# Optimization experiments

Hardware: AMD Instinct MI355X
Metric: run time of the kernel (lower is better)

Reference implementation:

```python
import jax, jax.numpy as jnp
import numpy as np

DIM = 768
HEADS = 12
HEAD_DIM = DIM // HEADS
SCALE = HEAD_DIM ** (-0.5)
GAMMA_INIT = 1.0


def _split_heads(x, B, H, Dh):
    # [B, N, C] -> [B, H, N, Dh]
    return x.reshape(B, -1, H, Dh).transpose(0, 2, 1, 3)


def setup_inputs() -> dict:
    key = jax.random.key(0)
    ks = jax.random.split(key, 10)
    B, N, C = 4, 1024, DIM
    w = lambda k: jax.random.normal(k, (C, C), dtype=jnp.float32) * 0.02
    return {
        "fc": jax.random.normal(ks[0], (B, N, C), dtype=jnp.float32),
        "fs": jax.random.normal(ks[1], (B, N, C), dtype=jnp.float32),
        "Wqc": w(ks[2]),
        "Wqs": w(ks[3]),
        "Wkc": w(ks[4]),
        "Wvc": w(ks[5]),
        "Wvs": w(ks[6]),
        "gamma": jnp.ones((HEADS,), dtype=jnp.float32) * GAMMA_INIT,
        "Wpc": w(ks[7]),
        "bpc": jnp.zeros((C,), dtype=jnp.float32),
        "Wps": w(ks[8]),
        "bps": jnp.zeros((C,), dtype=jnp.float32),
    }


def reference(fc, fs, Wqc, Wqs, Wkc, Wvc, Wvs, gamma, Wpc, bpc, Wps, bps):
    B, N, C = fc.shape
    H, Dh = HEADS, HEAD_DIM
    sg = jax.lax.stop_gradient

    qc = _split_heads(fc @ Wqc, B, H, Dh)
    qs = _split_heads(fs @ Wqs, B, H, Dh)
    kc = _split_heads(fc @ Wkc, B, H, Dh)
    vc = _split_heads(fc @ Wvc, B, H, Dh)
    vs = _split_heads(fs @ Wvs, B, H, Dh)

    # content attention: standard scaled QK^T
    attn_c = jnp.einsum("bhnd,bhmd->bhnm", qc, kc) * SCALE
    # semantic attention: L2-normalized self-similarity, per-head gamma
    qs_n = qs / jnp.linalg.norm(qs, axis=-1, keepdims=True)
    attn_s = jnp.einsum("bhnd,bhmd->bhnm", qs_n, qs_n) * gamma[None, :, None, None]

    # double softmax: identical forward values, asymmetric stop-gradients
    attn1 = jax.nn.softmax(attn_c + sg(attn_s), axis=-1)
    attn2 = jax.nn.softmax(sg(attn_c) + attn_s, axis=-1)

    oc = jnp.einsum("bhnm,bhmd->bhnd", attn1, vc).transpose(0, 2, 1, 3).reshape(B, N, C)
    os_ = jnp.einsum("bhnm,bhmd->bhnd", attn2, vs).transpose(0, 2, 1, 3).reshape(B, N, C)

    out_c = oc @ Wpc + bpc
    out_s = os_ @ Wps + bps
    return (out_c, out_s)
```

## Files before the change

kernel.cpp:

```cpp
#include <hip/hip_runtime.h>
#include <cstdint>
#include <cstddef>

#define DEV __device__ __forceinline__

typedef __bf16 v8bf __attribute__((ext_vector_type(8)));
typedef float v4f __attribute__((ext_vector_type(4)));
typedef float f32x16 __attribute__((ext_vector_type(16)));
typedef uint16_t u16;

DEV u16 f2bf(float f) {
    union { __bf16 b; u16 u; } cv;
    cv.b = (__bf16)f;
    return cv.u;
}
DEV float bf2f(u16 h) { return __uint_as_float((uint32_t)h << 16); }

DEV uint32_t pkbf(float a, float b) {
    typedef __bf16 bf2v __attribute__((ext_vector_type(2)));
    union { bf2v v; uint32_t u; } c;
    c.v = (bf2v){(__bf16)a, (__bf16)b};
    return c.u;
}

DEV void gload16(void* lds, const void* g) {
    __builtin_amdgcn_global_load_lds(
        (const __attribute__((address_space(1))) unsigned int*)g,
        (__attribute__((address_space(3))) unsigned int*)lds, 16, 0, 0);
}

DEV void wait_vm0() {
    asm volatile("s_waitcnt vmcnt(0)" ::: "memory");
    __builtin_amdgcn_sched_barrier(0);
}

__global__ __launch_bounds__(256) void k_cvt2(const float* __restrict__ a, const float* __restrict__ b,
                                              u16* __restrict__ da, u16* __restrict__ db) {
    const float* s = blockIdx.y ? b : a;
    u16* d = blockIdx.y ? db : da;
    int i = blockIdx.x * 256 + threadIdx.x;
    float4 v = reinterpret_cast<const float4*>(s)[i];
    ushort4 o;
    o.x = f2bf(v.x); o.y = f2bf(v.y); o.z = f2bf(v.z); o.w = f2bf(v.w);
    reinterpret_cast<ushort4*>(d)[i] = o;
}

__global__ __launch_bounds__(256) void k_transpose_w(
    const float* __restrict__ w0, const float* __restrict__ w1, const float* __restrict__ w2,
    const float* __restrict__ w3, const float* __restrict__ w4, const float* __restrict__ w5,
    const float* __restrict__ w6, u16* __restrict__ Wt) {
    __shared__ float tl[32][33];
    const float* W;
    switch (blockIdx.z) {
        case 0: W = w0; break; case 1: W = w1; break; case 2: W = w2; break;
        case 3: W = w3; break; case 4: W = w4; break; case 5: W = w5; break;
        default: W = w6; break;
    }
    int n0 = blockIdx.x * 32, k0 = blockIdx.y * 32;
    int tx = threadIdx.x & 31, ty = threadIdx.x >> 5;
    #pragma unroll
    for (int i = 0; i < 4; ++i)
        tl[ty + i*8][tx] = W[(size_t)(k0 + ty + i*8) * 768 + n0 + tx];
    __syncthreads();
    u16* O = Wt + (size_t)blockIdx.z * 589824;
    #pragma unroll
    for (int i = 0; i < 4; ++i)
        O[(size_t)(n0 + ty + i*8) * 768 + k0 + tx] = f2bf(tl[tx][ty + i*8]);
}

DEV void gemm_main(const u16* __restrict__ A, const u16* __restrict__ W,
                   u16* As, u16* Bs, int m0, int n0, v4f acc[4][4]) {
    const int t = threadIdx.x, lane = t & 63;
    const int wid = t >> 6, wm = wid >> 1, wn = wid & 1;
    const int lr = lane & 15, kg = lane >> 4;
    const int lrow = lane >> 3, lslot = lane & 7;
    const int s = lslot ^ lrow;
    #pragma unroll
    for (int mi = 0; mi < 4; ++mi)
        #pragma unroll
        for (int ni = 0; ni < 4; ++ni) acc[mi][ni] = (v4f){0.f, 0.f, 0.f, 0.f};
    for (int kt = 0; kt < 12; ++kt) {
        int k0 = kt * 64;
        #pragma unroll
        for (int c = 0; c < 4; ++c) {
            int rb = wid * 32 + c * 8;
            int r = rb + lrow;
            gload16((char*)As + rb * 128, A + (size_t)(m0 + r) * 768 + k0 + s * 8);
            gload16((char*)Bs + rb * 128, W + (size_t)(n0 + r) * 768 + k0 + s * 8);
        }
        __syncthreads();
        #pragma unroll
        for (int kk = 0; kk < 2; ++kk) {
            int kb2 = (kk * 32 + kg * 8) * 2;
            v8bf af[4], bfr[4];
            #pragma unroll
            for (int mi = 0; mi < 4; ++mi) {
                int rr = wm * 64 + mi * 16 + lr;
                af[mi] = *reinterpret_cast<const v8bf*>(reinterpret_cast<const char*>(As) + rr * 128 + (kb2 ^ ((rr & 7) << 4)));
            }
            #pragma unroll
            for (int ni = 0; ni < 4; ++ni) {
                int rr = wn * 64 + ni * 16 + lr;
                bfr[ni] = *reinterpret_cast<const v8bf*>(reinterpret_cast<const char*>(Bs) + rr * 128 + (kb2 ^ ((rr & 7) << 4)));
            }
            #pragma unroll
            for (int mi = 0; mi < 4; ++mi)
                #pragma unroll
                for (int ni = 0; ni < 4; ++ni)
                    acc[mi][ni] = __builtin_amdgcn_mfma_f32_16x16x32_bf16(af[mi], bfr[ni], acc[mi][ni], 0, 0, 0);
        }
        __syncthreads();
    }
}

__global__ __launch_bounds__(256) void k_gemm_proj(
    const u16* __restrict__ fcb, const u16* __restrict__ fsb, const u16* __restrict__ Wt,
    u16* __restrict__ qc, u16* __restrict__ kc, u16* __restrict__ vc,
    u16* __restrict__ qs, u16* __restrict__ vs) {
    __shared__ __align__(16) u16 As[8192], Bs[8192];
    const u16* A; const u16* W; u16* O;
    switch (blockIdx.z) {
        case 0:  A = fcb; W = Wt;              O = qc; break;
        case 1:  A = fcb; W = Wt + 589824;     O = kc; break;
        case 2:  A = fcb; W = Wt + 2 * 589824; O = vc; break;
        case 3:  A = fsb; W = Wt + 3 * 589824; O = qs; break;
        default: A = fsb; W = Wt + 4 * 589824; O = vs; break;
    }
    int m0 = blockIdx.y * 128, n0 = blockIdx.x * 128;
    v4f acc[4][4];
    gemm_main(A, W, As, Bs, m0, n0, acc);
    const int lane = threadIdx.x & 63, wid = threadIdx.x >> 6;
    const int wm = wid >> 1, wn = wid & 1, lr = lane & 15, kg = lane >> 4;
    if (blockIdx.z == 0) {
        #pragma unroll
        for (int mi = 0; mi < 4; ++mi)
            #pragma unroll
            for (int ni = 0; ni < 4; ++ni)
                #pragma unroll
                for (int r = 0; r < 4; ++r) acc[mi][ni][r] *= 0.18033688f;
    } else if (blockIdx.z == 3) {
        #pragma unroll
        for (int mi = 0; mi < 4; ++mi)
            #pragma unroll
            for (int r = 0; r < 4; ++r) {
                float ss = 0.f;
                #pragma unroll
                for (int ni = 0; ni < 4; ++ni) ss += acc[mi][ni][r] * acc[mi][ni][r];
                ss += __shfl_xor(ss, 1); ss += __shfl_xor(ss, 2);
                ss += __shfl_xor(ss, 4); ss += __shfl_xor(ss, 8);
                float rs = rsqrtf(ss);
                #pragma unroll
                for (int ni = 0; ni < 4; ++ni) acc[mi][ni][r] *= rs;
            }
    }
    #pragma unroll
    for (int mi = 0; mi < 4; ++mi)
        #pragma unroll
        for (int ni = 0; ni < 4; ++ni)
            #pragma unroll
            for (int r = 0; r < 4; ++r) {
                int rowg = m0 + wm * 64 + mi * 16 + kg * 4 + r;
                int colg = n0 + wn * 64 + ni * 16 + lr;
                O[(size_t)rowg * 768 + colg] = f2bf(acc[mi][ni][r]);
            }
}

__global__ __launch_bounds__(256) void k_gemm_out(
    const u16* __restrict__ ocb, const u16* __restrict__ osb, const u16* __restrict__ Wt,
    const float* __restrict__ bpc, const float* __restrict__ bps, float* __restrict__ out) {
    __shared__ __align__(16) u16 As[8192], Bs[8192];
    const u16* A; const u16* W; const float* bias; float* O;
    if (blockIdx.z == 0) { A = ocb; W = Wt + 5 * 589824; bias = bpc; O = out; }
    else                 { A = osb; W = Wt + 6 * 589824; bias = bps; O = out + 3145728; }
    int m0 = blockIdx.y * 128, n0 = blockIdx.x * 128;
    v4f acc[4][4];
    gemm_main(A, W, As, Bs, m0, n0, acc);
    const int lane = threadIdx.x & 63, wid = threadIdx.x >> 6;
    const int wm = wid >> 1, wn = wid & 1, lr = lane & 15, kg = lane >> 4;
    #pragma unroll
    for (int mi = 0; mi < 4; ++mi)
        #pragma unroll
        for (int ni = 0; ni < 4; ++ni)
            #pragma unroll
            for (int r = 0; r < 4; ++r) {
                int rowg = m0 + wm * 64 + mi * 16 + kg * 4 + r;
                int colg = n0 + wn * 64 + ni * 16 + lr;
                O[(size_t)rowg * 768 + colg] = acc[mi][ni][r] + bias[colg];
            }
}

__global__ __launch_bounds__(256) void k_transpose_v(
    const u16* __restrict__ vc, const u16* __restrict__ vs,
    u16* __restrict__ vcT, u16* __restrict__ vsT) {
    __shared__ u16 tile[64][65];
    const u16* src = blockIdx.z ? vs : vc;
    u16* dst = blockIdx.z ? vsT : vcT;
    int bh = blockIdx.y, b = bh / 12, h = bh % 12;
    int n0 = blockIdx.x * 64;
    int t = threadIdx.x;
    #pragma unroll
    for (int i = 0; i < 16; ++i) {
        int idx = i * 256 + t, n = idx >> 6, d = idx & 63;
        tile[n][d] = src[(size_t)(b * 1024 + n0 + n) * 768 + h * 64 + d];
    }
    __syncthreads();
    #pragma unroll
    for (int i = 0; i < 16; ++i) {
        int idx = i * 256 + t, d = idx >> 6, n = idx & 63;
        dst[(size_t)(bh * 64 + d) * 1024 + n0 + n] = tile[n][d];
    }
}

__global__ __launch_bounds__(256, 2) void k_attn(
    const u16* __restrict__ qc, const u16* __restrict__ kc, const u16* __restrict__ qsn,
    const u16* __restrict__ vcT, const u16* __restrict__ vsT,
    const float* __restrict__ gamma,
    u16* __restrict__ oc, u16* __restrict__ os) {
    __shared__ __align__(16) u16 SH[24576];
    u16* K_s8  = SH;
    u16* Q2_s8 = SH + 4096;
    u16* Vb    = SH + 8192;
    const int t = threadIdx.x, lane = t & 63, w = t >> 6;
    const int lq = lane & 31, hf = lane >> 5;
    const int qg = w >> 1, kvh = w & 1;
    const int lrow = lane >> 3, lslot = lane & 7;
    const int sslot = lslot ^ lrow;

    int lin = blockIdx.y * 16 + blockIdx.x;
    int swz = (lin & 7) * 96 + (lin >> 3);
    const int qb = swz & 15, bh = swz >> 4;
    const int b = bh / 12, h = bh % 12;
    const float gam = gamma[h] * 1.44269504088896340736f;

    const u16* gb; size_t rstride, kmul;
    switch (w) {
        case 0:  gb = kc  + (size_t)b * 786432 + h * 64; rstride = 768;  kmul = 768; break;
        case 1:  gb = qsn + (size_t)b * 786432 + h * 64; rstride = 768;  kmul = 768; break;
        case 2:  gb = vcT + (size_t)bh * 65536;          rstride = 1024; kmul = 1;   break;
        default: gb = vsT + (size_t)bh * 65536;          rstride = 1024; kmul = 1;   break;
    }
    u16* fixdst = (w == 0) ? K_s8 : Q2_s8;

    const u16* qp1 = qc  + (size_t)(b * 1024 + qb * 64 + qg * 32 + lq) * 768 + h * 64 + hf * 8;
    const u16* qp2 = qsn + (size_t)(b * 1024 + qb * 64 + qg * 32 + lq) * 768 + h * 64 + hf * 8;
    v8bf qcB[4], qsB[4];
    #pragma unroll
    for (int s = 0; s < 4; ++s) {
        qcB[s] = *reinterpret_cast<const v8bf*>(qp1 + s * 16);
        qsB[s] = *reinterpret_cast<const v8bf*>(qp2 + s * 16);
    }

    f32x16 ocA[2], osA[2];
    #pragma unroll
    for (int dt = 0; dt < 2; ++dt) {
        #pragma unroll
        for (int r = 0; r < 16; ++r) { ocA[dt][r] = 0.f; osA[dt][r] = 0.f; }
    }
    float lsum = 0.f;

    {
        char* ld = (w < 2) ? (char*)fixdst : (char*)(Vb + (w - 2) * 4096);
        #pragma unroll
        for (int c = 0; c < 8; ++c) {
            int r = c * 8 + lrow;
            gload16(ld + c * 1024, gb + (size_t)r * rstride + sslot * 8);
        }
    }
    wait_vm0();
    __builtin_amdgcn_s_barrier();

    int cur = 0;
    for (int tile = 0; tile < 16; ++tile) {
        if (tile < 15 && w >= 2) {
            size_t kv1 = (size_t)(tile + 1) * 64;
            char* ld = (char*)(Vb + ((cur ^ 1) * 2 + (w - 2)) * 4096);
            #pragma unroll
            for (int c = 0; c < 8; ++c) {
                int r = c * 8 + lrow;
                gload16(ld + c * 1024, gb + kv1 * kmul + (size_t)r * rstride + sslot * 8);
            }
        }
        const char* K_s  = (const char*)K_s8;
        const char* Q2_s = (const char*)Q2_s8;
        const char* Vc_s = (const char*)(Vb + (cur * 2 + 0) * 4096);
        const char* Vs_s = (const char*)(Vb + (cur * 2 + 1) * 4096);

        f32x16 ac, as;
        #pragma unroll
        for (int r = 0; r < 16; ++r) { ac[r] = 0.f; as[r] = 0.f; }
        const int rowA = kvh * 32 + lq;
        __builtin_amdgcn_s_setprio(1);
        #pragma unroll
        for (int s = 0; s < 4; ++s) {
            int colb = s * 32 + hf * 16;
            int off = rowA * 128 + (colb ^ ((rowA & 7) << 4));
            v8bf kf  = *reinterpret_cast<const v8bf*>(K_s + off);
            v8bf q2f = *reinterpret_cast<const v8bf*>(Q2_s + off);
            ac = __builtin_amdgcn_mfma_f32_32x32x16_bf16(kf,  qcB[s], ac, 0, 0, 0);
            as = __builtin_amdgcn_mfma_f32_32x32x16_bf16(q2f, qsB[s], as, 0, 0, 0);
        }
        __builtin_amdgcn_s_setprio(0);

        __builtin_amdgcn_s_barrier();
        if (tile < 15 && w < 2) {
            size_t kv1 = (size_t)(tile + 1) * 64;
            #pragma unroll
            for (int c = 0; c < 8; ++c) {
                int r = c * 8 + lrow;
                gload16((char*)fixdst + c * 1024, gb + kv1 * kmul + (size_t)r * rstride + sslot * 8);
            }
        }

        float p[16];
        #pragma unroll
        for (int r = 0; r < 16; ++r)
            p[r] = __builtin_exp2f(fmaf(gam, as[r], ac[r]));
        lsum += ((p[0]+p[1])+(p[2]+p[3])) + ((p[4]+p[5])+(p[6]+p[7]))
              + ((p[8]+p[9])+(p[10]+p[11])) + ((p[12]+p[13])+(p[14]+p[15]));

        uint32_t A0 = pkbf(p[0], p[1]),  A1 = pkbf(p[2], p[3]);
        uint32_t A2 = pkbf(p[4], p[5]),  A3 = pkbf(p[6], p[7]);
        uint32_t A4 = pkbf(p[8], p[9]),  A5 = pkbf(p[10], p[11]);
        uint32_t A6 = pkbf(p[12], p[13]), A7 = pkbf(p[14], p[15]);
        uint32_t pay0 = hf ? A0 : A2;
        uint32_t pay1 = hf ? A1 : A3;
        uint32_t rec0 = (uint32_t)__shfl_xor((int)pay0, 32);
        uint32_t rec1 = (uint32_t)__shfl_xor((int)pay1, 32);
        uint32_t w0 = hf ? rec0 : A0;
        uint32_t w1 = hf ? rec1 : A1;
        uint32_t w2 = hf ? A2 : rec0;
        uint32_t w3 = hf ? A3 : rec1;
        uint32_t pay2 = hf ? A4 : A6;
        uint32_t pay3 = hf ? A5 : A7;
        uint32_t rec2 = (uint32_t)__shfl_xor((int)pay2, 32);
        uint32_t rec3 = (uint32_t)__shfl_xor((int)pay3, 32);
        uint32_t w4 = hf ? rec2 : A4;
        uint32_t w5 = hf ? rec3 : A5;
        uint32_t w6 = hf ? A6 : rec2;
        uint32_t w7 = hf ? A7 : rec3;
        union { uint32_t u[4]; v8bf v; } pa0, pa1;
        pa0.u[0] = w0; pa0.u[1] = w1; pa0.u[2] = w2; pa0.u[3] = w3;
        pa1.u[0] = w4; pa1.u[1] = w5; pa1.u[2] = w6; pa1.u[3] = w7;

        __builtin_amdgcn_s_setprio(1);
        #pragma unroll
        for (int dt = 0; dt < 2; ++dt) {
            int rowV = dt * 32 + lq;
            #pragma unroll
            for (int s = 0; s < 2; ++s) {
                int colb = kvh * 64 + s * 32 + hf * 16;
                int off = rowV * 128 + (colb ^ ((rowV & 7) << 4));
                v8bf vcf = *reinterpret_cast<const v8bf*>(Vc_s + off);
                v8bf vsf = *reinterpret_cast<const v8bf*>(Vs_s + off);
                v8bf ap = s ? pa1.v : pa0.v;
                ocA[dt] = __builtin_amdgcn_mfma_f32_32x32x16_bf16(ap, vcf, ocA[dt], 0, 0, 0);
                osA[dt] = __builtin_amdgcn_mfma_f32_32x32x16_bf16(ap, vsf, osA[dt], 0, 0, 0);
            }
        }
        __builtin_amdgcn_s_setprio(0);

        wait_vm0();
        __builtin_amdgcn_s_barrier();
        cur ^= 1;
    }

    lsum += __shfl_xor(lsum, 32);
    float* red   = reinterpret_cast<float*>(SH);
    float* red_l = red;
    float* red_o = red + 64;
    if (kvh == 1) {
        if (lane < 32) red_l[qg * 32 + lq] = lsum;
        #pragma unroll
        for (int st = 0; st < 2; ++st)
            #pragma unroll
            for (int dt = 0; dt < 2; ++dt)
                #pragma unroll
                for (int r = 0; r < 16; ++r) {
                    int idx = st * 32 + dt * 16 + r;
                    float v = st ? osA[dt][r] : ocA[dt][r];
                    red_o[(qg * 64 + idx) * 64 + lane] = v;
                }
    }
    __syncthreads();
    if (kvh == 0) {
        float ltot = lsum + red_l[qg * 32 + lq];
        float rl = 1.0f / ltot;
        if (lane < 32) red_l[qg * 32 + lq] = rl;
        #pragma unroll
        for (int st = 0; st < 2; ++st)
            #pragma unroll
            for (int dt = 0; dt < 2; ++dt)
                #pragma unroll
                for (int r = 0; r < 16; ++r) {
                    int rowq = (r & 3) + 8 * (r >> 2) + 4 * hf;
                    float rlv = red_l[qg * 32 + rowq];
                    int idx = st * 32 + dt * 16 + r;
                    float own = st ? osA[dt][r] : ocA[dt][r];
                    float v = (own + red_o[(qg * 64 + idx) * 64 + lane]) * rlv;
                    u16* dst = st ? os : oc;
                    dst[(size_t)(b * 1024 + qb * 64 + qg * 32 + rowq) * 768 + h * 64 + dt * 32 + lq] = f2bf(v);
                }
    }
}

extern "C" void kernel_launch(void* const* d_in, const int* in_sizes, int n_in,
                              void* d_out, int out_size, void* d_ws, size_t ws_size,
                              hipStream_t stream) {
    const float* fc    = (const float*)d_in[0];
    const float* fs    = (const float*)d_in[1];
    const float* Wqc   = (const float*)d_in[2];
    const float* Wqs   = (const float*)d_in[3];
    const float* Wkc   = (const float*)d_in[4];
    const float* Wvc   = (const float*)d_in[5];
    const float* Wvs   = (const float*)d_in[6];
    const float* gamma = (const float*)d_in[7];
    const float* Wpc   = (const float*)d_in[8];
    const float* bpc   = (const float*)d_in[9];
    const float* Wps   = (const float*)d_in[10];
    const float* bps   = (const float*)d_in[11];
    float* out = (float*)d_out;

    const size_t NT = 3145728;
    u16* ws  = (u16*)d_ws;
    u16* fcb = ws;
    u16* fsb = fcb + NT;
    u16* Wt  = fsb + NT;
    u16* qc  = Wt + (size_t)7 * 589824;
    u16* kc  = qc + NT;
    u16* vc  = kc + NT;
    u16* qs  = vc + NT;
    u16* vs  = qs + NT;
    u16* vcT = vs + NT;
    u16* vsT = vcT + NT;
    u16* ocb = fcb;
    u16* osb = fsb;

    k_cvt2<<<dim3(3072, 2), 256, 0, stream>>>(fc, fs, fcb, fsb);
    k_transpose_w<<<dim3(24, 24, 7), 256, 0, stream>>>(Wqc, Wkc, Wvc, Wqs, Wvs, Wpc, Wps, Wt);
    k_gemm_proj<<<dim3(6, 32, 5), 256, 0, stream>>>(fcb, fsb, Wt, qc, kc, vc, qs, vs);
    k_transpose_v<<<dim3(16, 48, 2), 256, 0, stream>>>(vc, vs, vcT, vsT);
    k_attn<<<dim3(16, 48), 256, 0, stream>>>(qc, kc, qs, vcT, vsT, gamma, ocb, osb);
    k_gemm_out<<<dim3(6, 32, 2), 256, 0, stream>>>(ocb, osb, Wt, bpc, bps, out);
}
```

Baseline: 127.3 us.

## Merge input-convert and weight-transpose kernels; widen LDS swizzle in attention

Merges the activation bf16 conversion and the weight transpose into one launch with a flattened grid, which removes one kernel launch and lets the two jobs run together. In the attention kernel, the LDS swizzle for K/Q2/V tiles now also XORs bit 6 using row bit 3. The global-to-LDS load slot is permuted to match, so reads are meant to hit fewer LDS bank conflicts. The swizzle change has to stay consistent between the load side and the read side, otherwise the results are wrong.

```diff
diff --git a/kernel.cpp b/kernel.cpp
--- a/kernel.cpp
+++ b/kernel.cpp
@@ -14,7 +14,6 @@
     cv.b = (__bf16)f;
     return cv.u;
 }
-DEV float bf2f(u16 h) { return __uint_as_float((uint32_t)h << 16); }
 
 DEV uint32_t pkbf(float a, float b) {
     typedef __bf16 bf2v __attribute__((ext_vector_type(2)));
@@ -34,35 +33,40 @@
     __builtin_amdgcn_sched_barrier(0);
 }
 
-__global__ __launch_bounds__(256) void k_cvt2(const float* __restrict__ a, const float* __restrict__ b,
-                                              u16* __restrict__ da, u16* __restrict__ db) {
-    const float* s = blockIdx.y ? b : a;
-    u16* d = blockIdx.y ? db : da;
-    int i = blockIdx.x * 256 + threadIdx.x;
-    float4 v = reinterpret_cast<const float4*>(s)[i];
-    ushort4 o;
-    o.x = f2bf(v.x); o.y = f2bf(v.y); o.z = f2bf(v.z); o.w = f2bf(v.w);
-    reinterpret_cast<ushort4*>(d)[i] = o;
-}
-
-__global__ __launch_bounds__(256) void k_transpose_w(
+__global__ __launch_bounds__(256) void k_prep(
+    const float* __restrict__ fc, const float* __restrict__ fs,
+    u16* __restrict__ fcb, u16* __restrict__ fsb,
     const float* __restrict__ w0, const float* __restrict__ w1, const float* __restrict__ w2,
     const float* __restrict__ w3, const float* __restrict__ w4, const float* __restrict__ w5,
     const float* __restrict__ w6, u16* __restrict__ Wt) {
     __shared__ float tl[32][33];
+    int bid = blockIdx.x;
+    if (bid < 6144) {
+        const float* s = (bid < 3072) ? fc : fs;
+        u16* d = (bid < 3072) ? fcb : fsb;
+        int blk = (bid < 3072) ? bid : (bid - 3072);
+        int i = blk * 256 + threadIdx.x;
+        float4 v = reinterpret_cast<const float4*>(s)[i];
+        ushort4 o;
+        o.x = f2bf(v.x); o.y = f2bf(v.y); o.z = f2bf(v.z); o.w = f2bf(v.w);
+        reinterpret_cast<ushort4*>(d)[i] = o;
+        return;
+    }
+    int tid = bid - 6144;
+    int z = tid / 576, rem = tid % 576;
     const float* W;
-    switch (blockIdx.z) {
+    switch (z) {
         case 0: W = w0; break; case 1: W = w1; break; case 2: W = w2; break;
         case 3: W = w3; break; case 4: W = w4; break; case 5: W = w5; break;
         default: W = w6; break;
     }
-    int n0 = blockIdx.x * 32, k0 = blockIdx.y * 32;
+    int n0 = (rem % 24) * 32, k0 = (rem / 24) * 32;
     int tx = threadIdx.x & 31, ty = threadIdx.x >> 5;
     #pragma unroll
     for (int i = 0; i < 4; ++i)
         tl[ty + i*8][tx] = W[(size_t)(k0 + ty + i*8) * 768 + n0 + tx];
     __syncthreads();
-    u16* O = Wt + (size_t)blockIdx.z * 589824;
+    u16* O = Wt + (size_t)z * 589824;
     #pragma unroll
     for (int i = 0; i < 4; ++i)
         O[(size_t)(n0 + ty + i*8) * 768 + k0 + tx] = f2bf(tl[tx][ty + i*8]);
@@ -263,7 +267,8 @@
         #pragma unroll
         for (int c = 0; c < 8; ++c) {
             int r = c * 8 + lrow;
-            gload16(ld + c * 1024, gb + (size_t)r * rstride + sslot * 8);
+            int ss = sslot ^ ((c & 1) << 2);
+            gload16(ld + c * 1024, gb + (size_t)r * rstride + ss * 8);
         }
     }
     wait_vm0();
@@ -277,7 +282,8 @@
             #pragma unroll
             for (int c = 0; c < 8; ++c) {
                 int r = c * 8 + lrow;
-                gload16(ld + c * 1024, gb + kv1 * kmul + (size_t)r * rstride + sslot * 8);
+                int ss = sslot ^ ((c & 1) << 2);
+                gload16(ld + c * 1024, gb + kv1 * kmul + (size_t)r * rstride + ss * 8);
             }
         }
         const char* K_s  = (const char*)K_s8;
@@ -289,11 +295,12 @@
         #pragma unroll
         for (int r = 0; r < 16; ++r) { ac[r] = 0.f; as[r] = 0.f; }
         const int rowA = kvh * 32 + lq;
+        const int rswA = ((rowA & 7) << 4) ^ (((rowA >> 3) & 1) << 6);
         __builtin_amdgcn_s_setprio(1);
         #pragma unroll
         for (int s = 0; s < 4; ++s) {
             int colb = s * 32 + hf * 16;
-            int off = rowA * 128 + (colb ^ ((rowA & 7) << 4));
+            int off = rowA * 128 + (colb ^ rswA);
             v8bf kf  = *reinterpret_cast<const v8bf*>(K_s + off);
             v8bf q2f = *reinterpret_cast<const v8bf*>(Q2_s + off);
             ac = __builtin_amdgcn_mfma_f32_32x32x16_bf16(kf,  qcB[s], ac, 0, 0, 0);
@@ -307,7 +314,8 @@
             #pragma unroll
             for (int c = 0; c < 8; ++c) {
                 int r = c * 8 + lrow;
-                gload16((char*)fixdst + c * 1024, gb + kv1 * kmul + (size_t)r * rstride + sslot * 8);
+                int ss = sslot ^ ((c & 1) << 2);
+                gload16((char*)fixdst + c * 1024, gb + kv1 * kmul + (size_t)r * rstride + ss * 8);
             }
         }
 
@@ -346,10 +354,11 @@
         #pragma unroll
         for (int dt = 0; dt < 2; ++dt) {
             int rowV = dt * 32 + lq;
+            int rswV = ((rowV & 7) << 4) ^ (((rowV >> 3) & 1) << 6);
             #pragma unroll
             for (int s = 0; s < 2; ++s) {
                 int colb = kvh * 64 + s * 32 + hf * 16;
-                int off = rowV * 128 + (colb ^ ((rowV & 7) << 4));
+                int off = rowV * 128 + (colb ^ rswV);
                 v8bf vcf = *reinterpret_cast<const v8bf*>(Vc_s + off);
                 v8bf vsf = *reinterpret_cast<const v8bf*>(Vs_s + off);
                 v8bf ap = s ? pa1.v : pa0.v;
@@ -435,8 +444,7 @@
     u16* ocb = fcb;
     u16* osb = fsb;
 
-    k_cvt2<<<dim3(3072, 2), 256, 0, stream>>>(fc, fs, fcb, fsb);
-    k_transpose_w<<<dim3(24, 24, 7), 256, 0, stream>>>(Wqc, Wkc, Wvc, Wqs, Wvs, Wpc, Wps, Wt);
+    k_prep<<<10176, 256, 0, stream>>>(fc, fs, fcb, fsb, Wqc, Wkc, Wvc, Wqs, Wvs, Wpc, Wps, Wt);
     k_gemm_proj<<<dim3(6, 32, 5), 256, 0, stream>>>(fcb, fsb, Wt, qc, kc, vc, qs, vs);
     k_transpose_v<<<dim3(16, 48, 2), 256, 0, stream>>>(vc, vs, vcT, vsT);
     k_attn<<<dim3(16, 48), 256, 0, stream>>>(qc, kc, qs, vcT, vsT, gamma, ocb, osb);
```

Result: no change. 125.3 us, median of 3 (-1.6%).
